# Performance work log

Measured on AMD Instinct MI355X. Metric: run time of the kernel, lower is better.

## Reference

```python
import jax, jax.numpy as jnp
import numpy as np

B, N, S, NS, V = 4, 4096, 1024, 32, 8
CIN, COUT = 64, 128
RADIUS = 0.2
C1 = CIN + 6  # cin + grouped_xyz(3) + local_xyz(3)
EPS = 1e-5


def _bn(x, g, b):
    # training-mode batchnorm over all axes except the trailing channel axis
    axes = tuple(range(x.ndim - 1))
    m = jnp.mean(x, axes, keepdims=True)
    v = jnp.var(x, axes, keepdims=True)
    return (x - m) * jax.lax.rsqrt(v + EPS) * g + b


def _fps(xyz, s):
    # farthest point sampling, deterministic start at index 0
    b, n, _ = xyz.shape
    bar = jnp.arange(b)
    def step(carry, _):
        mind, last = carry
        p = xyz[bar, last]  # [B,3]
        d = jnp.sum((xyz - p[:, None, :]) ** 2, -1)
        mind = jnp.minimum(mind, d)
        nxt = jnp.argmax(mind, -1).astype(jnp.int32)
        return (mind, nxt), nxt
    idx0 = jnp.zeros((b,), jnp.int32)
    _, rest = jax.lax.scan(step, (jnp.full((b, n), 1e10, xyz.dtype), idx0), None, length=s - 1)
    idx = jnp.concatenate([idx0[None], rest], 0).T  # [B,S]
    return jnp.take_along_axis(xyz, idx[..., None], axis=1), idx


def _ball_query(new_xyz, xyz, k, radius):
    # first-k-in-index-order points within radius; -1 padding like pytorch3d
    n = xyz.shape[1]
    d2 = jnp.sum((new_xyz[:, :, None, :] - xyz[:, None, :, :]) ** 2, -1)  # [B,S,N]
    key = jnp.where(d2 < radius * radius, jnp.arange(n, dtype=jnp.int32), n)
    negk, _ = jax.lax.top_k(-key, k)  # k smallest keys
    idx = -negk
    mask = idx >= n
    return jnp.where(mask, -1, idx), mask


def _masked_gather(x, idx):
    # gather rows of x [B,N,C] at idx [B,S,k]; zeros where idx == -1
    b, s, k = idx.shape
    safe = jnp.maximum(idx, 0).reshape(b, s * k)
    g = jnp.take_along_axis(x, safe[..., None], axis=1).reshape(b, s, k, x.shape[-1])
    return jnp.where((idx == -1)[..., None], 0.0, g)


def setup_inputs() -> dict:
    key = jax.random.key(0)
    ks = jax.random.split(key, 10)
    xyz = jax.random.uniform(ks[0], (B, N, 3), jnp.float32)
    f = jax.random.normal(ks[1], (B, N, CIN), jnp.float32)
    # cube-corner frame points, scaled by radius*0.8, rotated about Y (as in __init__)
    corners = jnp.array([[x, y, z] for x in (-1.0, 1.0) for y in (-1.0, 1.0) for z in (-1.0, 1.0)], jnp.float32)
    ang = jax.random.uniform(ks[2], ()) * 2.0 * jnp.pi
    c, sn = jnp.cos(ang), jnp.sin(ang)
    z, o = jnp.zeros(()), jnp.ones(())
    rot = jnp.stack([jnp.stack([c, z, sn]), jnp.stack([z, o, z]), jnp.stack([-sn, z, c])])
    framepoints = (corners * (RADIUS * 0.8)) @ rot.T
    w = lambda k_, sh: jax.random.normal(k_, sh, jnp.float32) * 0.05
    return {
        "xyz": xyz, "f": f, "framepoints": framepoints,
        "w1_0": w(ks[3], (13, 64)), "b1_0": jnp.zeros((64,), jnp.float32),
        "g1_0": jnp.ones((64,), jnp.float32), "bt1_0": jnp.zeros((64,), jnp.float32),
        "w1_1": w(ks[4], (64, C1)), "b1_1": jnp.zeros((C1,), jnp.float32),
        "w2_0": w(ks[5], (C1, 128)), "b2_0": jnp.zeros((128,), jnp.float32),
        "g2_0": jnp.ones((128,), jnp.float32), "bt2_0": jnp.zeros((128,), jnp.float32),
        "w2_1": w(ks[6], (128, COUT)), "b2_1": jnp.zeros((COUT,), jnp.float32),
        "res_w": w(ks[7], (CIN, COUT)), "res_b": jnp.zeros((COUT,), jnp.float32),
    }


def _forward(xyz, f, framepoints, w1_0, b1_0, g1_0, bt1_0, w1_1, b1_1,
             w2_0, b2_0, g2_0, bt2_0, w2_1, b2_1, res_w, res_b):
    new_xyz, _ = _fps(xyz, S)                           # [B,S,3]
    idx, mask = _ball_query(new_xyz, xyz, NS, RADIUS)   # [B,S,NS]
    grouped_xyz = _masked_gather(xyz, idx)              # [B,S,NS,3]
    grouped_feature = _masked_gather(f, idx)            # [B,S,NS,CIN]
    local = grouped_xyz - new_xyz[:, :, None, :]
    gf = jnp.concatenate([grouped_xyz, local, grouped_feature], -1)   # [B,S,NS,C1]
    arrow = grouped_xyz[:, :, :, None, :] - framepoints               # [B,S,NS,V,3]
    euc = jnp.sqrt(jnp.sum(arrow ** 2, -1, keepdims=True))
    gx = jnp.broadcast_to(grouped_xyz[:, :, :, None, :], arrow.shape)
    fp = jnp.broadcast_to(framepoints, arrow.shape)
    coc = jnp.concatenate([-arrow, arrow, euc, gx, fp], -1)           # [B,S,NS,V,13]
    # m1: per-point MLP (1x1x1 Conv3d) 13 -> 64 (bn+relu) -> C1
    a = jax.nn.relu(_bn(coc @ w1_0 + b1_0, g1_0, bt1_0))
    a = a @ w1_1 + b1_1                                               # [B,S,NS,V,C1]
    # frame-modulated features + softmax attention over the V frame axis
    p = gf[:, :, :, None, :] * a                                      # [B,S,NS,V,C1]
    agg = jnp.sum(jax.nn.softmax(p, axis=3) * p, axis=3)              # [B,S,NS,C1]
    agg = jnp.where(mask[..., None], 0.0, agg)
    # m2: per-point MLP (1x1 Conv2d) C1 -> 128 (bn+relu) -> COUT
    wmid = jax.nn.relu(_bn(agg @ w2_0 + b2_0, g2_0, bt2_0))
    wout = wmid @ w2_1 + b2_1                                         # [B,S,NS,COUT]
    new_f = jax.nn.gelu(wout + grouped_feature @ res_w + res_b, approximate=False)
    return jnp.max(new_f, axis=2), new_xyz


def reference(xyz, f, framepoints, w1_0, b1_0, g1_0, bt1_0, w1_1, b1_1,
              w2_0, b2_0, g2_0, bt2_0, w2_1, b2_1, res_w, res_b):
    return _forward(xyz, f, framepoints, w1_0, b1_0, g1_0, bt1_0, w1_1, b1_1,
                    w2_0, b2_0, g2_0, bt2_0, w2_1, b2_1, res_w, res_b)
```

## Files before the change

kernel.cpp:

```cpp
#include <hip/hip_runtime.h>
#include <hip/hip_bf16.h>
#include <math.h>

typedef __hip_bfloat16 bf16;
typedef __attribute__((ext_vector_type(8))) short short8;
typedef __attribute__((ext_vector_type(4))) float f32x4;

#define BB  4
#define NN  4096
#define SS  1024
#define KNS 32
#define C1  70

__device__ __forceinline__ float b2f(bf16 x){ return __bfloat162float(x); }

__device__ __forceinline__ float ld(const void* p, size_t i, bool F){
    return F ? ((const float*)p)[i] : __bfloat162float(((const bf16*)p)[i]);
}
__device__ __forceinline__ void st(void* p, size_t i, float v, bool F){
    if (F) ((float*)p)[i] = v; else ((bf16*)p)[i] = __float2bfloat16(v);
}
__device__ __forceinline__ unsigned short f2us(float x){
    __hip_bfloat16 h = __float2bfloat16(x);
    return *reinterpret_cast<unsigned short*>(&h);
}
__device__ __forceinline__ float us2f(unsigned short u){
    return __uint_as_float(((unsigned)u) << 16);
}

__global__ void init_kernel(const void* xyz, double* __restrict__ M,
                            double* __restrict__ sums, int* __restrict__ flag){
    __shared__ int cnt;
    const int t = threadIdx.x;
    if (t == 0) cnt = 0;
    if (t < 105) M[t] = 0.0;
    if (t < 256) sums[t] = 0.0;
    __syncthreads();
    int c = 0;
    for (int i = t; i < 2048; i += 256){
        float v = __bfloat162float(((const bf16*)xyz)[i]);
        if (!(fabsf(v) <= 1.5f)) c++;
    }
    atomicAdd(&cnt, c);
    __syncthreads();
    if (t == 0) *flag = (cnt > 10) ? 1 : 0;
}

__global__ __launch_bounds__(256) void fps_kernel(const void* __restrict__ xyz,
        float* __restrict__ nxf, void* __restrict__ out, const int* __restrict__ flag){
    __shared__ float4 pts[NN];
    __shared__ int sidx[SS];
    __shared__ unsigned long long skey[2][4];
    const bool F = (*flag != 0);
    const int b = blockIdx.x, t = threadIdx.x, lane = t & 63, w = t >> 6;
    float px[16], py[16], pz[16], mind[16];
#pragma unroll
    for (int j = 0; j < 16; j++){
        int i = j*256 + t;
        float X = ld(xyz, (size_t)(b*NN+i)*3+0, F);
        float Y = ld(xyz, (size_t)(b*NN+i)*3+1, F);
        float Z = ld(xyz, (size_t)(b*NN+i)*3+2, F);
        px[j] = X; py[j] = Y; pz[j] = Z; mind[j] = 1e10f;
        pts[i] = make_float4(X, Y, Z, 0.f);
    }
    if (t == 0) sidx[0] = 0;
    __syncthreads();
    float4 q = pts[0];
    for (int s = 1; s < SS; s++){
        float bd = -1.f; int bi = 0;
#pragma unroll
        for (int j = 0; j < 16; j++){
            float dx = __fsub_rn(px[j], q.x);
            float dy = __fsub_rn(py[j], q.y);
            float dz = __fsub_rn(pz[j], q.z);
            float d  = __fadd_rn(__fadd_rn(__fmul_rn(dx,dx), __fmul_rn(dy,dy)), __fmul_rn(dz,dz));
            float m = fminf(mind[j], d); mind[j] = m;
            if (m > bd){ bd = m; bi = j*256 + t; }
        }
        unsigned long long key = ((unsigned long long)__float_as_uint(bd) << 32)
                               | (unsigned)(~bi);
#pragma unroll
        for (int off = 1; off < 64; off <<= 1){
            unsigned long long o = __shfl_xor(key, off);
            if (o > key) key = o;
        }
        const int par = s & 1;
        if (lane == 0) skey[par][w] = key;
        __syncthreads();
        unsigned long long k0 = skey[par][0], k1 = skey[par][1];
        unsigned long long k2 = skey[par][2], k3 = skey[par][3];
        if (k1 > k0) k0 = k1;
        if (k3 > k2) k2 = k3;
        if (k2 > k0) k0 = k2;
        int ix = (int)(~(unsigned)(k0 & 0xffffffffull));
        if (t == 0) sidx[s] = ix;
        q = pts[ix];
    }
    __syncthreads();
    const size_t o1 = (size_t)BB*SS*128;
    for (int s2 = t; s2 < SS; s2 += 256){
        int i = sidx[s2];
        float4 p = pts[i];
        nxf[(b*SS+s2)*3+0] = p.x; nxf[(b*SS+s2)*3+1] = p.y; nxf[(b*SS+s2)*3+2] = p.z;
        st(out, o1 + (size_t)(b*SS+s2)*3+0, p.x, F);
        st(out, o1 + (size_t)(b*SS+s2)*3+1, p.y, F);
        st(out, o1 + (size_t)(b*SS+s2)*3+2, p.z, F);
    }
}

__global__ __launch_bounds__(512) void ball_kernel(const void* __restrict__ xyz,
        const float* __restrict__ nxf, int* __restrict__ idx, const int* __restrict__ flag){
    __shared__ float sx[NN], sy[NN], sz[NN];
    const bool F = (*flag != 0);
    const int b = blockIdx.x, t = threadIdx.x, lane = t & 63, w = t >> 6;
    for (int i = t; i < NN; i += 512){
        sx[i] = ld(xyz, (size_t)(b*NN+i)*3+0, F);
        sy[i] = ld(xyz, (size_t)(b*NN+i)*3+1, F);
        sz[i] = ld(xyz, (size_t)(b*NN+i)*3+2, F);
    }
    __syncthreads();
    const float R2 = 0.2f*0.2f;
    const unsigned long long below = (lane == 63) ? ~0ull >> 1
                                   : ((1ull << lane) - 1ull);
#pragma unroll
    for (int cc = 0; cc < 4; cc++){
        const int s = blockIdx.y*32 + w*4 + cc;
        const float px = nxf[(b*SS+s)*3+0];
        const float py = nxf[(b*SS+s)*3+1];
        const float pz = nxf[(b*SS+s)*3+2];
        int* op = idx + (size_t)(b*SS+s)*KNS;
        int cnt = 0;
        for (int c = 0; c < 64; c++){
            const int i = c*64 + lane;
            float dx = __fsub_rn(px, sx[i]);
            float dy = __fsub_rn(py, sy[i]);
            float dz = __fsub_rn(pz, sz[i]);
            float d2 = __fadd_rn(__fadd_rn(__fmul_rn(dx,dx), __fmul_rn(dy,dy)), __fmul_rn(dz,dz));
            const bool hit = (d2 < R2);
            unsigned long long m = __ballot(hit);
            if (hit){
                int pos = cnt + __popcll(m & below);
                if (pos < KNS) op[pos] = i;
            }
            cnt += __popcll(m);
            if (cnt >= KNS) break;
        }
        if (lane < KNS && lane >= cnt) op[lane] = -1;
    }
}

__global__ __launch_bounds__(256) void bn1_stats(const void* __restrict__ xyz,
        const int* __restrict__ idx, const void* __restrict__ fpt, double* __restrict__ M,
        const int* __restrict__ flag){
    __shared__ float sfp[24];
    const bool F = (*flag != 0);
    const int t = threadIdx.x, lane = t & 63;
    if (t < 24) sfp[t] = ld(fpt, t, F);
    __syncthreads();
    float acc[105];
#pragma unroll
    for (int q = 0; q < 105; q++) acc[q] = 0.f;
    for (int it = 0; it < 8; it++){
        const int row = blockIdx.x*2048 + it*256 + t;
        const int b = row >> 15;
        const int id = idx[row];
        float gx = 0.f, gy = 0.f, gz = 0.f;
        if (id >= 0){
            gx = ld(xyz, (size_t)(b*NN+id)*3+0, F);
            gy = ld(xyz, (size_t)(b*NN+id)*3+1, F);
            gz = ld(xyz, (size_t)(b*NN+id)*3+2, F);
        }
#pragma unroll
        for (int v = 0; v < 8; v++){
            float fxv = sfp[v*3+0], fyv = sfp[v*3+1], fzv = sfp[v*3+2];
            float ax = gx - fxv, ay = gy - fyv, az = gz - fzv;
            float eu = sqrtf(ax*ax + ay*ay + az*az);
            float fv[14];
            fv[0] = -ax; fv[1] = -ay; fv[2] = -az;
            fv[3] =  ax; fv[4] =  ay; fv[5] =  az;
            fv[6] = eu;  fv[7] = gx;  fv[8] = gy; fv[9] = gz;
            fv[10] = fxv; fv[11] = fyv; fv[12] = fzv; fv[13] = 1.0f;
            int q = 0;
#pragma unroll
            for (int i = 0; i < 14; i++)
#pragma unroll
                for (int j = i; j < 14; j++){
                    acc[q] = fmaf(fv[i], fv[j], acc[q]);
                    q++;
                }
        }
    }
#pragma unroll
    for (int q = 0; q < 105; q++){
        float s = acc[q];
#pragma unroll
        for (int off = 1; off < 64; off <<= 1) s += __shfl_xor(s, off);
        if (lane == 0) atomicAdd(&M[q], (double)s);
    }
}

__global__ __launch_bounds__(128) void bn1_final(const double* __restrict__ M,
        const void* __restrict__ w10, const void* __restrict__ b10,
        const void* __restrict__ g1, const void* __restrict__ bt1, float* __restrict__ bn1,
        const int* __restrict__ flag){
    __shared__ double Mm[14][14];
    __shared__ double mv[14];
    const bool F = (*flag != 0);
    const int t = threadIdx.x;
    if (t < 105){
        int e = t, i = 0, off = 0;
        while (e - off >= 14 - i){ off += 14 - i; i++; }
        int j = i + (e - off);
        double val = M[t];
        Mm[i][j] = val; Mm[j][i] = val;
    }
    __syncthreads();
    const double K = 1048576.0;
    if (t < 14) mv[t] = Mm[t][13] / K;
    __syncthreads();
    if (t < 64){
        double wc[13];
        for (int i = 0; i < 13; i++) wc[i] = (double)ld(w10, i*64+t, F);
        double mean = (double)ld(b10, t, F);
        for (int i = 0; i < 13; i++) mean += mv[i]*wc[i];
        double var = 0.0;
        for (int i = 0; i < 13; i++)
            for (int j = 0; j < 13; j++)
                var += wc[i]*wc[j]*(Mm[i][j]/K - mv[i]*mv[j]);
        float sc = ld(g1, t, F) / sqrtf((float)var + 1e-5f);
        bn1[t] = sc;
        bn1[64+t] = ld(bt1, t, F) - (float)mean * sc;
    }
}

__global__ __launch_bounds__(256) void m1_kernel(
        const void* __restrict__ xyz, const void* __restrict__ f, const void* __restrict__ fpt,
        const void* __restrict__ w10, const void* __restrict__ b10,
        const void* __restrict__ w11, const void* __restrict__ b11,
        const float* __restrict__ nxf, const int* __restrict__ idx,
        const float* __restrict__ bn1, float* __restrict__ agg, const int* __restrict__ flag){
    __shared__ short sthi[4*2*8*72];
    __shared__ short stlo[4*2*8*72];
    __shared__ float gfb[4*2*80];
    const bool F = (*flag != 0);
    const int t = threadIdx.x, lane = t & 63, w = t >> 6;
    const int kq = lane >> 4, cn = lane & 15;

    short8 Bh[2][5], Bl[2][5];
#pragma unroll
    for (int ks = 0; ks < 2; ks++)
#pragma unroll
    for (int nt = 0; nt < 5; nt++){
        short8 bh, bl;
#pragma unroll
        for (int j = 0; j < 8; j++){
            int k = ks*32 + kq*8 + j;
            int c = nt*16 + cn;
            float wv = (c < C1) ? ld(w11, (size_t)k*C1 + c, F) : 0.f;
            unsigned short h = f2us(wv);
            unsigned short l2 = f2us(wv - us2f(h));
            bh[j] = (short)h; bl[j] = (short)l2;
        }
        Bh[ks][nt] = bh; Bl[ks][nt] = bl;
    }
    float binit[5];
#pragma unroll
    for (int nt = 0; nt < 5; nt++){
        int c = nt*16 + cn;
        binit[nt] = (c < C1) ? ld(b11, c, F) : 0.f;
    }
    float W10c[13];
#pragma unroll
    for (int i = 0; i < 13; i++) W10c[i] = ld(w10, i*64+lane, F);
    const float b10v = ld(b10, lane, F);
    const float sc1 = bn1[lane], sh1 = bn1[64+lane];
    float fx[8], fy[8], fz[8];
#pragma unroll
    for (int v = 0; v < 8; v++){
        fx[v] = ld(fpt, v*3+0, F); fy[v] = ld(fpt, v*3+1, F); fz[v] = ld(fpt, v*3+2, F);
    }
    const int quad = lane >> 4;
    const int rr = quad >> 1;
    const int hh = quad & 1;
    const int mA = lane & 15;
    const int rA = mA >> 3, vA = mA & 7;

    const int wid = blockIdx.x*4 + w;
    for (int p = 0; p < 16; p++){
        const int rowbase = wid*32 + p*2;
        int ids[2];
#pragma unroll
        for (int r = 0; r < 2; r++){
            const int row = rowbase + r;
            const int b = row >> 15, s = (row >> 5) & 1023;
            const int id = idx[row];
            ids[r] = id;
            float gx = 0.f, gy = 0.f, gz = 0.f, fv0 = 0.f, fv1 = 0.f;
            if (id >= 0){
                gx = ld(xyz, (size_t)(b*NN+id)*3+0, F);
                gy = ld(xyz, (size_t)(b*NN+id)*3+1, F);
                gz = ld(xyz, (size_t)(b*NN+id)*3+2, F);
                if (lane >= 6) fv0 = ld(f, (size_t)(b*NN+id)*64 + (lane-6), F);
                if (lane < 6)  fv1 = ld(f, (size_t)(b*NN+id)*64 + (58+lane), F);
            }
            const float nxx = nxf[(b*SS+s)*3+0], nxy = nxf[(b*SS+s)*3+1], nxz = nxf[(b*SS+s)*3+2];
            float gf0;
            if (lane == 0) gf0 = gx; else if (lane == 1) gf0 = gy; else if (lane == 2) gf0 = gz;
            else if (lane == 3) gf0 = gx - nxx; else if (lane == 4) gf0 = gy - nxy;
            else if (lane == 5) gf0 = gz - nxz; else gf0 = fv0;
            gfb[w*160 + r*80 + lane] = gf0;
            if (lane < 6)       gfb[w*160 + r*80 + 64 + lane] = fv1;
            else if (lane < 16) gfb[w*160 + r*80 + 64 + lane] = 0.f;
            const int sb = ((w*2 + r)*8)*72 + lane;
#pragma unroll
            for (int v = 0; v < 8; v++){
                float ax = gx - fx[v], ay = gy - fy[v], az = gz - fz[v];
                float eu = sqrtf(ax*ax + ay*ay + az*az);
                float z = b10v;
                z = fmaf(-ax, W10c[0], z); z = fmaf(-ay, W10c[1], z); z = fmaf(-az, W10c[2], z);
                z = fmaf( ax, W10c[3], z); z = fmaf( ay, W10c[4], z); z = fmaf( az, W10c[5], z);
                z = fmaf( eu, W10c[6], z);
                z = fmaf( gx, W10c[7], z); z = fmaf( gy, W10c[8], z); z = fmaf( gz, W10c[9], z);
                z = fmaf(fx[v], W10c[10], z); z = fmaf(fy[v], W10c[11], z); z = fmaf(fz[v], W10c[12], z);
                float a1 = fmaxf(fmaf(z, sc1, sh1), 0.f);
                unsigned short h = f2us(a1);
                unsigned short l2 = f2us(a1 - us2f(h));
                sthi[sb + v*72] = (short)h;
                stlo[sb + v*72] = (short)l2;
            }
        }
        f32x4 acc[5];
#pragma unroll
        for (int nt = 0; nt < 5; nt++){
            f32x4 a; a[0] = binit[nt]; a[1] = binit[nt]; a[2] = binit[nt]; a[3] = binit[nt];
            acc[nt] = a;
        }
        const int aoff = ((w*2 + rA)*8 + vA)*72 + kq*8;
#pragma unroll
        for (int ks = 0; ks < 2; ks++){
            short8 ahi = *(const short8*)&sthi[aoff + ks*32];
            short8 alo = *(const short8*)&stlo[aoff + ks*32];
#pragma unroll
            for (int nt = 0; nt < 5; nt++){
                acc[nt] = __builtin_amdgcn_mfma_f32_16x16x32_bf16(ahi, Bh[ks][nt], acc[nt], 0, 0, 0);
                acc[nt] = __builtin_amdgcn_mfma_f32_16x16x32_bf16(alo, Bh[ks][nt], acc[nt], 0, 0, 0);
                acc[nt] = __builtin_amdgcn_mfma_f32_16x16x32_bf16(ahi, Bl[ks][nt], acc[nt], 0, 0, 0);
            }
        }
        const bool msk = ((rr == 0 ? ids[0] : ids[1]) < 0);
#pragma unroll
        for (int nt = 0; nt < 5; nt++){
            const int col = nt*16 + cn;
            float gfv = gfb[w*160 + rr*80 + col];
            f32x4 a = acc[nt];
            float p0 = a[0]*gfv, p1 = a[1]*gfv, p2 = a[2]*gfv, p3 = a[3]*gfv;
            float mx = fmaxf(fmaxf(p0, p1), fmaxf(p2, p3));
            mx = fmaxf(mx, __shfl_xor(mx, 16));
            float e0 = __expf(p0 - mx), e1 = __expf(p1 - mx);
            float e2 = __expf(p2 - mx), e3 = __expf(p3 - mx);
            float den4 = (e0 + e1) + (e2 + e3);
            float num4 = fmaf(e3, p3, fmaf(e2, p2, fmaf(e1, p1, e0*p0)));
            float den = den4 + __shfl_xor(den4, 16);
            float num = num4 + __shfl_xor(num4, 16);
            float outv = num / den;
            if (hh == 0 && col < C1){
                agg[(size_t)(rowbase + rr)*C1 + col] = msk ? 0.f : outv;
            }
        }
    }
}

__global__ __launch_bounds__(256) void prep1_kernel(
        const void* __restrict__ w20, const void* __restrict__ w21,
        const void* __restrict__ rw, const void* __restrict__ b20,
        const void* __restrict__ b21, const void* __restrict__ rb,
        float* __restrict__ w20r, float* __restrict__ w21f, float* __restrict__ rwf,
        float* __restrict__ b20r, float* __restrict__ bof, const int* __restrict__ flag){
    const bool F = (*flag != 0);
    int e = blockIdx.x*256 + threadIdx.x;
    if (e < 8960){ w20r[e] = ld(w20, e, F); return; }
    int e2 = e - 8960;
    if (e2 < 16384){ w21f[e2] = ld(w21, e2, F); return; }
    int e3 = e2 - 16384;
    if (e3 < 8192){ rwf[e3] = ld(rw, e3, F); return; }
    int e4 = e3 - 8192;
    if (e4 < 128){
        b20r[e4] = ld(b20, e4, F);
        bof[e4]  = ld(b21, e4, F) + ld(rb, e4, F);
    }
}

__global__ __launch_bounds__(256) void bn2_stats(const float* __restrict__ agg,
        const float* __restrict__ w20r, const float* __restrict__ b20r,
        double* __restrict__ sums){
    __shared__ float aggT[70*65];
    const int t = threadIdx.x, lane = t & 63;
    const int wbase = __builtin_amdgcn_readfirstlane((t >> 6) << 5);
    float binit[32];
#pragma unroll
    for (int j = 0; j < 32; j++) binit[j] = b20r[wbase + j];
    float accs[32], accq[32];
#pragma unroll
    for (int j = 0; j < 32; j++){ accs[j] = 0.f; accq[j] = 0.f; }
    for (int it = 0; it < 8; it++){
        const int rowbase = blockIdx.x*512 + it*64;
        __syncthreads();
        for (int e = t; e < 70*64; e += 256){
            int r = e / 70, k = e - r*70;
            aggT[k*65 + r] = agg[(size_t)rowbase*70 + e];
        }
        __syncthreads();
        float z[32];
#pragma unroll
        for (int j = 0; j < 32; j++) z[j] = binit[j];
#pragma unroll 2
        for (int k = 0; k < 70; k++){
            float av = aggT[k*65 + lane];
            const float* wr = w20r + k*128 + wbase;
#pragma unroll
            for (int j = 0; j < 32; j++) z[j] = fmaf(av, wr[j], z[j]);
        }
#pragma unroll
        for (int j = 0; j < 32; j++){
            accs[j] += z[j];
            accq[j] = fmaf(z[j], z[j], accq[j]);
        }
    }
#pragma unroll
    for (int j = 0; j < 32; j++){
        float s = accs[j], q = accq[j];
#pragma unroll
        for (int off = 1; off < 64; off <<= 1){
            s += __shfl_xor(s, off);
            q += __shfl_xor(q, off);
        }
        if (lane == 0){
            atomicAdd(&sums[wbase + j], (double)s);
            atomicAdd(&sums[128 + wbase + j], (double)q);
        }
    }
}

__global__ void bn2_final(const double* __restrict__ sums, const void* __restrict__ g2,
        const void* __restrict__ bt2, float* __restrict__ bn2, const int* __restrict__ flag){
    const bool F = (*flag != 0);
    int t = threadIdx.x;
    const double K = 131072.0;
    double mean = sums[t] / K;
    double var = sums[128+t] / K - mean*mean;
    float sc = ld(g2, t, F) / sqrtf((float)var + 1e-5f);
    bn2[t] = sc;
    bn2[128+t] = ld(bt2, t, F) - (float)mean * sc;
}

__global__ __launch_bounds__(256) void prep2_kernel(
        const float* __restrict__ w20r, const float* __restrict__ b20r,
        const float* __restrict__ bn2,
        float* __restrict__ w20f, float* __restrict__ b20f){
    int e = blockIdx.x*256 + threadIdx.x;
    if (e < 8960){ w20f[e] = w20r[e] * bn2[e & 127]; return; }
    int e2 = e - 8960;
    if (e2 < 128){ b20f[e2] = b20r[e2]*bn2[e2] + bn2[128+e2]; }
}

__global__ __launch_bounds__(256) void final_kernel(
        const float* __restrict__ agg, const void* __restrict__ f, const int* __restrict__ idx,
        const float* __restrict__ w20f, const float* __restrict__ b20f,
        const float* __restrict__ w21f, const float* __restrict__ rwf,
        const float* __restrict__ bof,
        void* __restrict__ out, const int* __restrict__ flag){
    __shared__ float aggT[70*65];
    __shared__ float gfs[64*65];
    __shared__ float wmids[128*64];
    __shared__ float obuf[256];
    const bool F = (*flag != 0);
    const int t = threadIdx.x, lane = t & 63;
    const int wbase = __builtin_amdgcn_readfirstlane((t >> 6) << 5);
    const int rowbase = blockIdx.x * 64;
    for (int e = t; e < 70*64; e += 256){
        int r = e / 70, k = e - r*70;
        aggT[k*65 + r] = agg[(size_t)rowbase*70 + e];
    }
    for (int e = t; e < 64*64; e += 256){
        int r = e >> 6, cin = e & 63;
        int id = idx[rowbase + r];
        int b = (rowbase + r) >> 15;
        gfs[cin*65 + r] = (id >= 0) ? ld(f, (size_t)(b*NN+id)*64 + cin, F) : 0.f;
    }
    __syncthreads();
    float acc[32];
#pragma unroll
    for (int j = 0; j < 32; j++) acc[j] = b20f[wbase + j];
#pragma unroll 2
    for (int k = 0; k < 70; k++){
        float av = aggT[k*65 + lane];
        const float* wr = w20f + k*128 + wbase;
#pragma unroll
        for (int j = 0; j < 32; j++) acc[j] = fmaf(av, wr[j], acc[j]);
    }
#pragma unroll
    for (int j = 0; j < 32; j++)
        wmids[(wbase + j)*64 + lane] = fmaxf(acc[j], 0.f);
    __syncthreads();
    float acc2[32];
#pragma unroll
    for (int j = 0; j < 32; j++) acc2[j] = bof[wbase + j];
#pragma unroll 2
    for (int k = 0; k < 128; k++){
        float wv = wmids[k*64 + lane];
        const float* wr = w21f + k*128 + wbase;
#pragma unroll
        for (int j = 0; j < 32; j++) acc2[j] = fmaf(wv, wr[j], acc2[j]);
    }
#pragma unroll 2
    for (int k = 0; k < 64; k++){
        float gv = gfs[k*65 + lane];
        const float* wr = rwf + k*128 + wbase;
#pragma unroll
        for (int j = 0; j < 32; j++) acc2[j] = fmaf(gv, wr[j], acc2[j]);
    }
#pragma unroll
    for (int j = 0; j < 32; j++){
        float x = acc2[j];
        float y = 0.5f * x * (1.f + erff(x * 0.70710678118654752f));
#pragma unroll
        for (int off = 1; off < 32; off <<= 1)
            y = fmaxf(y, __shfl_xor(y, off));
        if ((lane & 31) == 0) obuf[(lane >> 5)*128 + wbase + j] = y;
    }
    __syncthreads();
    st(out, (size_t)blockIdx.x*256 + t, obuf[t], F);
}

extern "C" void kernel_launch(void* const* d_in, const int* in_sizes, int n_in,
                              void* d_out, int out_size, void* d_ws, size_t ws_size,
                              hipStream_t stream){
    const void* xyz = d_in[0];
    const void* f   = d_in[1];
    const void* fpt = d_in[2];
    const void* w10 = d_in[3];
    const void* b10 = d_in[4];
    const void* g1  = d_in[5];
    const void* bt1 = d_in[6];
    const void* w11 = d_in[7];
    const void* b11 = d_in[8];
    const void* w20 = d_in[9];
    const void* b20 = d_in[10];
    const void* g2  = d_in[11];
    const void* bt2 = d_in[12];
    const void* w21 = d_in[13];
    const void* b21 = d_in[14];
    const void* rw  = d_in[15];
    const void* rb  = d_in[16];

    char* ws = (char*)d_ws;
    float*  nxf  = (float*) (ws + 0);
    int*    idx  = (int*)   (ws + 65536);
    double* M    = (double*)(ws + 655360);
    float*  bn1  = (float*) (ws + 786432);
    double* sums = (double*)(ws + 917504);
    float*  bn2  = (float*) (ws + 1048576);
    int*    flag = (int*)   (ws + 1050624);
    float*  w20f = (float*) (ws + 1114112);
    float*  w21f = (float*) (ws + 1179648);
    float*  rwf  = (float*) (ws + 1245184);
    float*  b20f = (float*) (ws + 1277952);
    float*  bof  = (float*) (ws + 1278464);
    float*  w20r = (float*) (ws + 1310720);
    float*  b20r = (float*) (ws + 1441792);
    float*  agg  = (float*) (ws + 2097152);

    init_kernel<<<1, 256, 0, stream>>>(xyz, M, sums, flag);
    fps_kernel<<<4, 256, 0, stream>>>(xyz, nxf, d_out, flag);
    ball_kernel<<<dim3(4, 32), 512, 0, stream>>>(xyz, nxf, idx, flag);
    prep1_kernel<<<132, 256, 0, stream>>>(w20, w21, rw, b20, b21, rb,
                                          w20r, w21f, rwf, b20r, bof, flag);
    bn1_stats<<<64, 256, 0, stream>>>(xyz, idx, fpt, M, flag);
    bn1_final<<<1, 128, 0, stream>>>(M, w10, b10, g1, bt1, bn1, flag);
    m1_kernel<<<1024, 256, 0, stream>>>(xyz, f, fpt, w10, b10, w11, b11, nxf, idx, bn1, agg, flag);
    bn2_stats<<<256, 256, 0, stream>>>(agg, w20r, b20r, sums);
    bn2_final<<<1, 128, 0, stream>>>(sums, g2, bt2, bn2, flag);
    prep2_kernel<<<36, 256, 0, stream>>>(w20r, b20r, bn2, w20f, b20f);
    final_kernel<<<2048, 256, 0, stream>>>(agg, f, idx, w20f, b20f, w21f, rwf, bof, d_out, flag);
}
```

Baseline: 1.467 ms.

## Move bn2_stats and final MLP GEMMs to split-bf16 MFMA, shrink bn1 moments

The fp32 scalar FMA GEMMs in bn2_stats and final_kernel become 16x16x32 bf16 MFMA ops. Each fp32 operand is split into hi and lo bf16 parts and three products are summed, keeping near-fp32 accuracy. Weights are pre-packed into MFMA fragment layout in prep1/prep2. bn1_stats now accumulates a deduplicated 11-feature second-moment matrix instead of 14, with signs remapped in bn1_final, and uses more blocks with fewer rows each. The cost is three MFMAs per tile and bf16-split rounding error.

```diff
diff --git a/kernel.cpp b/kernel.cpp
--- a/kernel.cpp
+++ b/kernel.cpp
@@ -157,11 +157,11 @@
     const int t = threadIdx.x, lane = t & 63;
     if (t < 24) sfp[t] = ld(fpt, t, F);
     __syncthreads();
-    float acc[105];
-#pragma unroll
-    for (int q = 0; q < 105; q++) acc[q] = 0.f;
-    for (int it = 0; it < 8; it++){
-        const int row = blockIdx.x*2048 + it*256 + t;
+    float acc[66];
+#pragma unroll
+    for (int q = 0; q < 66; q++) acc[q] = 0.f;
+    for (int it = 0; it < 4; it++){
+        const int row = blockIdx.x*1024 + it*256 + t;
         const int b = row >> 15;
         const int id = idx[row];
         float gx = 0.f, gy = 0.f, gz = 0.f;
@@ -175,23 +175,22 @@
             float fxv = sfp[v*3+0], fyv = sfp[v*3+1], fzv = sfp[v*3+2];
             float ax = gx - fxv, ay = gy - fyv, az = gz - fzv;
             float eu = sqrtf(ax*ax + ay*ay + az*az);
-            float fv[14];
-            fv[0] = -ax; fv[1] = -ay; fv[2] = -az;
-            fv[3] =  ax; fv[4] =  ay; fv[5] =  az;
-            fv[6] = eu;  fv[7] = gx;  fv[8] = gy; fv[9] = gz;
-            fv[10] = fxv; fv[11] = fyv; fv[12] = fzv; fv[13] = 1.0f;
+            float f11[11];
+            f11[0] = ax; f11[1] = ay; f11[2] = az; f11[3] = eu;
+            f11[4] = gx; f11[5] = gy; f11[6] = gz;
+            f11[7] = fxv; f11[8] = fyv; f11[9] = fzv; f11[10] = 1.0f;
             int q = 0;
 #pragma unroll
-            for (int i = 0; i < 14; i++)
-#pragma unroll
-                for (int j = i; j < 14; j++){
-                    acc[q] = fmaf(fv[i], fv[j], acc[q]);
+            for (int i = 0; i < 11; i++)
+#pragma unroll
+                for (int j = i; j < 11; j++){
+                    acc[q] = fmaf(f11[i], f11[j], acc[q]);
                     q++;
                 }
         }
     }
 #pragma unroll
-    for (int q = 0; q < 105; q++){
+    for (int q = 0; q < 66; q++){
         float s = acc[q];
 #pragma unroll
         for (int off = 1; off < 64; off <<= 1) s += __shfl_xor(s, off);
@@ -203,30 +202,34 @@
         const void* __restrict__ w10, const void* __restrict__ b10,
         const void* __restrict__ g1, const void* __restrict__ bt1, float* __restrict__ bn1,
         const int* __restrict__ flag){
-    __shared__ double Mm[14][14];
-    __shared__ double mv[14];
+    __shared__ double Ms[11][11];
+    __shared__ double mv14[14];
     const bool F = (*flag != 0);
     const int t = threadIdx.x;
-    if (t < 105){
+    if (t < 66){
         int e = t, i = 0, off = 0;
-        while (e - off >= 14 - i){ off += 14 - i; i++; }
+        while (e - off >= 11 - i){ off += 11 - i; i++; }
         int j = i + (e - off);
         double val = M[t];
-        Mm[i][j] = val; Mm[j][i] = val;
+        Ms[i][j] = val; Ms[j][i] = val;
     }
     __syncthreads();
     const double K = 1048576.0;
-    if (t < 14) mv[t] = Mm[t][13] / K;
+    const int    bi14[14] = {0,1,2, 0,1,2, 3, 4,5,6, 7,8,9, 10};
+    const double sg14[14] = {-1,-1,-1, 1,1,1, 1, 1,1,1, 1,1,1, 1};
+    if (t < 14) mv14[t] = sg14[t] * Ms[bi14[t]][10] / K;
     __syncthreads();
     if (t < 64){
         double wc[13];
         for (int i = 0; i < 13; i++) wc[i] = (double)ld(w10, i*64+t, F);
         double mean = (double)ld(b10, t, F);
-        for (int i = 0; i < 13; i++) mean += mv[i]*wc[i];
+        for (int i = 0; i < 13; i++) mean += mv14[i]*wc[i];
         double var = 0.0;
         for (int i = 0; i < 13; i++)
-            for (int j = 0; j < 13; j++)
-                var += wc[i]*wc[j]*(Mm[i][j]/K - mv[i]*mv[j]);
+            for (int j = 0; j < 13; j++){
+                double mij = sg14[i]*sg14[j]*Ms[bi14[i]][bi14[j]]/K;
+                var += wc[i]*wc[j]*(mij - mv14[i]*mv14[j]);
+            }
         float sc = ld(g1, t, F) / sqrtf((float)var + 1e-5f);
         bn1[t] = sc;
         bn1[64+t] = ld(bt1, t, F) - (float)mean * sc;
@@ -370,73 +373,107 @@
     }
 }
 
+__device__ __forceinline__ void pack_frag(int e, int K, const void* W, bool F, float scale,
+                                          short* H, short* L){
+    int j = e & 7, lane = (e >> 3) & 63, nt = (e >> 9) & 7, kt = e >> 12;
+    int k = kt*32 + ((lane >> 4) & 3)*8 + j;
+    int n = nt*16 + (lane & 15);
+    float v = (k < K) ? ld(W, (size_t)k*128 + n, F) * scale : 0.f;
+    unsigned short h = f2us(v);
+    unsigned short l2 = f2us(v - us2f(h));
+    H[e] = (short)h; L[e] = (short)l2;
+}
+
 __global__ __launch_bounds__(256) void prep1_kernel(
         const void* __restrict__ w20, const void* __restrict__ w21,
         const void* __restrict__ rw, const void* __restrict__ b20,
         const void* __restrict__ b21, const void* __restrict__ rb,
-        float* __restrict__ w20r, float* __restrict__ w21f, float* __restrict__ rwf,
+        short* __restrict__ w20rp_h, short* __restrict__ w20rp_l,
+        short* __restrict__ w21p_h, short* __restrict__ w21p_l,
+        short* __restrict__ rwp_h, short* __restrict__ rwp_l,
         float* __restrict__ b20r, float* __restrict__ bof, const int* __restrict__ flag){
     const bool F = (*flag != 0);
     int e = blockIdx.x*256 + threadIdx.x;
-    if (e < 8960){ w20r[e] = ld(w20, e, F); return; }
-    int e2 = e - 8960;
-    if (e2 < 16384){ w21f[e2] = ld(w21, e2, F); return; }
-    int e3 = e2 - 16384;
-    if (e3 < 8192){ rwf[e3] = ld(rw, e3, F); return; }
-    int e4 = e3 - 8192;
-    if (e4 < 128){
-        b20r[e4] = ld(b20, e4, F);
-        bof[e4]  = ld(b21, e4, F) + ld(rb, e4, F);
+    if (e < 12288){ pack_frag(e, 70, w20, F, 1.f, w20rp_h, w20rp_l); return; }
+    e -= 12288;
+    if (e < 16384){ pack_frag(e, 128, w21, F, 1.f, w21p_h, w21p_l); return; }
+    e -= 16384;
+    if (e < 8192){ pack_frag(e, 64, rw, F, 1.f, rwp_h, rwp_l); return; }
+    e -= 8192;
+    if (e < 128){
+        b20r[e] = ld(b20, e, F);
+        bof[e]  = ld(b21, e, F) + ld(rb, e, F);
     }
 }
 
 __global__ __launch_bounds__(256) void bn2_stats(const float* __restrict__ agg,
-        const float* __restrict__ w20r, const float* __restrict__ b20r,
-        double* __restrict__ sums){
-    __shared__ float aggT[70*65];
-    const int t = threadIdx.x, lane = t & 63;
-    const int wbase = __builtin_amdgcn_readfirstlane((t >> 6) << 5);
-    float binit[32];
-#pragma unroll
-    for (int j = 0; j < 32; j++) binit[j] = b20r[wbase + j];
-    float accs[32], accq[32];
-#pragma unroll
-    for (int j = 0; j < 32; j++){ accs[j] = 0.f; accq[j] = 0.f; }
+        const short* __restrict__ w20rp_h, const short* __restrict__ w20rp_l,
+        const float* __restrict__ b20r, double* __restrict__ sums){
+    __shared__ short Xh[64*104];
+    __shared__ short Xl[64*104];
+    const int t = threadIdx.x, lane = t & 63, w = t >> 6;
+    const int cn = lane & 15, kq = lane >> 4;
+    for (int e = t; e < 64*34; e += 256){
+        int r = e/34, k = 70 + (e - r*34);
+        Xh[r*104+k] = 0; Xl[r*104+k] = 0;
+    }
+    float bias[8];
+#pragma unroll
+    for (int nt = 0; nt < 8; nt++) bias[nt] = b20r[nt*16 + cn];
+    f32x4 accS[8], accQ[8];
+#pragma unroll
+    for (int nt = 0; nt < 8; nt++){
+        f32x4 zz; zz[0]=0.f; zz[1]=0.f; zz[2]=0.f; zz[3]=0.f;
+        accS[nt] = zz; accQ[nt] = zz;
+    }
     for (int it = 0; it < 8; it++){
         const int rowbase = blockIdx.x*512 + it*64;
         __syncthreads();
-        for (int e = t; e < 70*64; e += 256){
-            int r = e / 70, k = e - r*70;
-            aggT[k*65 + r] = agg[(size_t)rowbase*70 + e];
+        for (int e = t; e < 64*70; e += 256){
+            int r = e/70, k = e - r*70;
+            float v = agg[(size_t)rowbase*70 + e];
+            unsigned short h = f2us(v);
+            unsigned short l2 = f2us(v - us2f(h));
+            Xh[r*104+k] = (short)h; Xl[r*104+k] = (short)l2;
         }
         __syncthreads();
-        float z[32];
-#pragma unroll
-        for (int j = 0; j < 32; j++) z[j] = binit[j];
-#pragma unroll 2
-        for (int k = 0; k < 70; k++){
-            float av = aggT[k*65 + lane];
-            const float* wr = w20r + k*128 + wbase;
-#pragma unroll
-            for (int j = 0; j < 32; j++) z[j] = fmaf(av, wr[j], z[j]);
-        }
-#pragma unroll
-        for (int j = 0; j < 32; j++){
-            accs[j] += z[j];
-            accq[j] = fmaf(z[j], z[j], accq[j]);
-        }
-    }
-#pragma unroll
-    for (int j = 0; j < 32; j++){
-        float s = accs[j], q = accq[j];
-#pragma unroll
-        for (int off = 1; off < 64; off <<= 1){
-            s += __shfl_xor(s, off);
-            q += __shfl_xor(q, off);
-        }
-        if (lane == 0){
-            atomicAdd(&sums[wbase + j], (double)s);
-            atomicAdd(&sums[128 + wbase + j], (double)q);
+        f32x4 z[8];
+#pragma unroll
+        for (int nt = 0; nt < 8; nt++){
+            f32x4 a; a[0]=bias[nt]; a[1]=bias[nt]; a[2]=bias[nt]; a[3]=bias[nt];
+            z[nt] = a;
+        }
+#pragma unroll
+        for (int kt = 0; kt < 3; kt++){
+            short8 Ah = *(const short8*)&Xh[(w*16 + cn)*104 + kt*32 + kq*8];
+            short8 Al = *(const short8*)&Xl[(w*16 + cn)*104 + kt*32 + kq*8];
+#pragma unroll
+            for (int nt = 0; nt < 8; nt++){
+                short8 Wh = ((const short8*)w20rp_h)[(kt*8+nt)*64 + lane];
+                short8 Wl = ((const short8*)w20rp_l)[(kt*8+nt)*64 + lane];
+                z[nt] = __builtin_amdgcn_mfma_f32_16x16x32_bf16(Ah, Wh, z[nt], 0, 0, 0);
+                z[nt] = __builtin_amdgcn_mfma_f32_16x16x32_bf16(Al, Wh, z[nt], 0, 0, 0);
+                z[nt] = __builtin_amdgcn_mfma_f32_16x16x32_bf16(Ah, Wl, z[nt], 0, 0, 0);
+            }
+        }
+#pragma unroll
+        for (int nt = 0; nt < 8; nt++){
+#pragma unroll
+            for (int rg = 0; rg < 4; rg++){
+                accS[nt][rg] += z[nt][rg];
+                accQ[nt][rg] = fmaf(z[nt][rg], z[nt][rg], accQ[nt][rg]);
+            }
+        }
+    }
+#pragma unroll
+    for (int nt = 0; nt < 8; nt++){
+        float s = (accS[nt][0] + accS[nt][1]) + (accS[nt][2] + accS[nt][3]);
+        float q = (accQ[nt][0] + accQ[nt][1]) + (accQ[nt][2] + accQ[nt][3]);
+        s += __shfl_xor(s, 16); s += __shfl_xor(s, 32);
+        q += __shfl_xor(q, 16); q += __shfl_xor(q, 32);
+        if (lane < 16){
+            atomicAdd(&sums[nt*16 + cn], (double)s);
+            atomicAdd(&sums[128 + nt*16 + cn], (double)q);
         }
     }
 }
@@ -454,82 +491,149 @@
 }
 
 __global__ __launch_bounds__(256) void prep2_kernel(
-        const float* __restrict__ w20r, const float* __restrict__ b20r,
+        const void* __restrict__ w20, const float* __restrict__ b20r,
         const float* __restrict__ bn2,
-        float* __restrict__ w20f, float* __restrict__ b20f){
+        short* __restrict__ w20p_h, short* __restrict__ w20p_l,
+        float* __restrict__ b20f, const int* __restrict__ flag){
+    const bool F = (*flag != 0);
     int e = blockIdx.x*256 + threadIdx.x;
-    if (e < 8960){ w20f[e] = w20r[e] * bn2[e & 127]; return; }
-    int e2 = e - 8960;
-    if (e2 < 128){ b20f[e2] = b20r[e2]*bn2[e2] + bn2[128+e2]; }
+    if (e < 12288){
+        int j = e & 7, lane = (e >> 3) & 63, nt = (e >> 9) & 7, kt = e >> 12;
+        int k = kt*32 + ((lane >> 4) & 3)*8 + j;
+        int n = nt*16 + (lane & 15);
+        float v = (k < 70) ? ld(w20, (size_t)k*128 + n, F) * bn2[n] : 0.f;
+        unsigned short h = f2us(v);
+        unsigned short l2 = f2us(v - us2f(h));
+        w20p_h[e] = (short)h; w20p_l[e] = (short)l2;
+        return;
+    }
+    e -= 12288;
+    if (e < 128) b20f[e] = b20r[e]*bn2[e] + bn2[128+e];
 }
 
 __global__ __launch_bounds__(256) void final_kernel(
         const float* __restrict__ agg, const void* __restrict__ f, const int* __restrict__ idx,
-        const float* __restrict__ w20f, const float* __restrict__ b20f,
-        const float* __restrict__ w21f, const float* __restrict__ rwf,
+        const short* __restrict__ w20p_h, const short* __restrict__ w20p_l,
+        const float* __restrict__ b20f,
+        const short* __restrict__ w21p_h, const short* __restrict__ w21p_l,
+        const short* __restrict__ rwp_h, const short* __restrict__ rwp_l,
         const float* __restrict__ bof,
         void* __restrict__ out, const int* __restrict__ flag){
-    __shared__ float aggT[70*65];
-    __shared__ float gfs[64*65];
-    __shared__ float wmids[128*64];
-    __shared__ float obuf[256];
-    const bool F = (*flag != 0);
-    const int t = threadIdx.x, lane = t & 63;
-    const int wbase = __builtin_amdgcn_readfirstlane((t >> 6) << 5);
+    __shared__ short Xh[64*104];
+    __shared__ short Xl[64*104];
+    __shared__ short Yh[64*152];
+    __shared__ short Yl[64*152];
+    __shared__ float obuf[4][128];
+    const bool F = (*flag != 0);
+    const int t = threadIdx.x, lane = t & 63, w = t >> 6;
+    const int cn = lane & 15, kq = lane >> 4;
     const int rowbase = blockIdx.x * 64;
-    for (int e = t; e < 70*64; e += 256){
-        int r = e / 70, k = e - r*70;
-        aggT[k*65 + r] = agg[(size_t)rowbase*70 + e];
+    for (int e = t; e < 64*34; e += 256){
+        int r = e/34, k = 70 + (e - r*34);
+        Xh[r*104+k] = 0; Xl[r*104+k] = 0;
+    }
+    for (int e = t; e < 64*70; e += 256){
+        int r = e/70, k = e - r*70;
+        float v = agg[(size_t)rowbase*70 + e];
+        unsigned short h = f2us(v);
+        unsigned short l2 = f2us(v - us2f(h));
+        Xh[r*104+k] = (short)h; Xl[r*104+k] = (short)l2;
+    }
+    __syncthreads();
+    f32x4 z[8];
+#pragma unroll
+    for (int nt = 0; nt < 8; nt++){
+        float b = b20f[nt*16 + cn];
+        f32x4 a; a[0]=b; a[1]=b; a[2]=b; a[3]=b;
+        z[nt] = a;
+    }
+#pragma unroll
+    for (int kt = 0; kt < 3; kt++){
+        short8 Ah = *(const short8*)&Xh[(w*16 + cn)*104 + kt*32 + kq*8];
+        short8 Al = *(const short8*)&Xl[(w*16 + cn)*104 + kt*32 + kq*8];
+#pragma unroll
+        for (int nt = 0; nt < 8; nt++){
+            short8 Wh = ((const short8*)w20p_h)[(kt*8+nt)*64 + lane];
+            short8 Wl = ((const short8*)w20p_l)[(kt*8+nt)*64 + lane];
+            z[nt] = __builtin_amdgcn_mfma_f32_16x16x32_bf16(Ah, Wh, z[nt], 0, 0, 0);
+            z[nt] = __builtin_amdgcn_mfma_f32_16x16x32_bf16(Al, Wh, z[nt], 0, 0, 0);
+            z[nt] = __builtin_amdgcn_mfma_f32_16x16x32_bf16(Ah, Wl, z[nt], 0, 0, 0);
+        }
+    }
+    __syncthreads();
+#pragma unroll
+    for (int nt = 0; nt < 8; nt++){
+#pragma unroll
+        for (int rg = 0; rg < 4; rg++){
+            float y = fmaxf(z[nt][rg], 0.f);
+            unsigned short h = f2us(y);
+            unsigned short l2 = f2us(y - us2f(h));
+            int row = w*16 + kq*4 + rg, col = nt*16 + cn;
+            Yh[row*152+col] = (short)h; Yl[row*152+col] = (short)l2;
+        }
     }
     for (int e = t; e < 64*64; e += 256){
-        int r = e >> 6, cin = e & 63;
+        int r = e >> 6, k = e & 63;
         int id = idx[rowbase + r];
         int b = (rowbase + r) >> 15;
-        gfs[cin*65 + r] = (id >= 0) ? ld(f, (size_t)(b*NN+id)*64 + cin, F) : 0.f;
-    }
-    __syncthreads();
-    float acc[32];
-#pragma unroll
-    for (int j = 0; j < 32; j++) acc[j] = b20f[wbase + j];
-#pragma unroll 2
-    for (int k = 0; k < 70; k++){
-        float av = aggT[k*65 + lane];
-        const float* wr = w20f + k*128 + wbase;
-#pragma unroll
-        for (int j = 0; j < 32; j++) acc[j] = fmaf(av, wr[j], acc[j]);
-    }
-#pragma unroll
-    for (int j = 0; j < 32; j++)
-        wmids[(wbase + j)*64 + lane] = fmaxf(acc[j], 0.f);
-    __syncthreads();
-    float acc2[32];
-#pragma unroll
-    for (int j = 0; j < 32; j++) acc2[j] = bof[wbase + j];
-#pragma unroll 2
-    for (int k = 0; k < 128; k++){
-        float wv = wmids[k*64 + lane];
-        const float* wr = w21f + k*128 + wbase;
-#pragma unroll
-        for (int j = 0; j < 32; j++) acc2[j] = fmaf(wv, wr[j], acc2[j]);
-    }
-#pragma unroll 2
-    for (int k = 0; k < 64; k++){
-        float gv = gfs[k*65 + lane];
-        const float* wr = rwf + k*128 + wbase;
-#pragma unroll
-        for (int j = 0; j < 32; j++) acc2[j] = fmaf(gv, wr[j], acc2[j]);
-    }
-#pragma unroll
-    for (int j = 0; j < 32; j++){
-        float x = acc2[j];
-        float y = 0.5f * x * (1.f + erff(x * 0.70710678118654752f));
-#pragma unroll
-        for (int off = 1; off < 32; off <<= 1)
-            y = fmaxf(y, __shfl_xor(y, off));
-        if ((lane & 31) == 0) obuf[(lane >> 5)*128 + wbase + j] = y;
-    }
-    __syncthreads();
-    st(out, (size_t)blockIdx.x*256 + t, obuf[t], F);
+        float v = (id >= 0) ? ld(f, (size_t)(b*NN+id)*64 + k, F) : 0.f;
+        unsigned short h = f2us(v);
+        unsigned short l2 = f2us(v - us2f(h));
+        Xh[r*88+k] = (short)h; Xl[r*88+k] = (short)l2;
+    }
+    __syncthreads();
+    f32x4 acc2[8];
+#pragma unroll
+    for (int nt = 0; nt < 8; nt++){
+        float b = bof[nt*16 + cn];
+        f32x4 a; a[0]=b; a[1]=b; a[2]=b; a[3]=b;
+        acc2[nt] = a;
+    }
+#pragma unroll
+    for (int kt = 0; kt < 4; kt++){
+        short8 Ah = *(const short8*)&Yh[(w*16 + cn)*152 + kt*32 + kq*8];
+        short8 Al = *(const short8*)&Yl[(w*16 + cn)*152 + kt*32 + kq*8];
+#pragma unroll
+        for (int nt = 0; nt < 8; nt++){
+            short8 Wh = ((const short8*)w21p_h)[(kt*8+nt)*64 + lane];
+            short8 Wl = ((const short8*)w21p_l)[(kt*8+nt)*64 + lane];
+            acc2[nt] = __builtin_amdgcn_mfma_f32_16x16x32_bf16(Ah, Wh, acc2[nt], 0, 0, 0);
+            acc2[nt] = __builtin_amdgcn_mfma_f32_16x16x32_bf16(Al, Wh, acc2[nt], 0, 0, 0);
+            acc2[nt] = __builtin_amdgcn_mfma_f32_16x16x32_bf16(Ah, Wl, acc2[nt], 0, 0, 0);
+        }
+    }
+#pragma unroll
+    for (int kt = 0; kt < 2; kt++){
+        short8 Ah = *(const short8*)&Xh[(w*16 + cn)*88 + kt*32 + kq*8];
+        short8 Al = *(const short8*)&Xl[(w*16 + cn)*88 + kt*32 + kq*8];
+#pragma unroll
+        for (int nt = 0; nt < 8; nt++){
+            short8 Wh = ((const short8*)rwp_h)[(kt*8+nt)*64 + lane];
+            short8 Wl = ((const short8*)rwp_l)[(kt*8+nt)*64 + lane];
+            acc2[nt] = __builtin_amdgcn_mfma_f32_16x16x32_bf16(Ah, Wh, acc2[nt], 0, 0, 0);
+            acc2[nt] = __builtin_amdgcn_mfma_f32_16x16x32_bf16(Al, Wh, acc2[nt], 0, 0, 0);
+            acc2[nt] = __builtin_amdgcn_mfma_f32_16x16x32_bf16(Ah, Wl, acc2[nt], 0, 0, 0);
+        }
+    }
+#pragma unroll
+    for (int nt = 0; nt < 8; nt++){
+        float m = -3.4e38f;
+#pragma unroll
+        for (int rg = 0; rg < 4; rg++){
+            float x = acc2[nt][rg];
+            float y = 0.5f * x * (1.f + erff(x * 0.70710678118654752f));
+            m = fmaxf(m, y);
+        }
+        m = fmaxf(m, __shfl_xor(m, 16));
+        m = fmaxf(m, __shfl_xor(m, 32));
+        if (lane < 16) obuf[w][nt*16 + cn] = m;
+    }
+    __syncthreads();
+    {
+        int g = t >> 7, c = t & 127;
+        float y = fmaxf(obuf[2*g][c], obuf[2*g+1][c]);
+        st(out, (size_t)blockIdx.x*256 + t, y, F);
+    }
 }
 
 extern "C" void kernel_launch(void* const* d_in, const int* in_sizes, int n_in,
@@ -554,32 +658,38 @@
     const void* rb  = d_in[16];
 
     char* ws = (char*)d_ws;
-    float*  nxf  = (float*) (ws + 0);
-    int*    idx  = (int*)   (ws + 65536);
-    double* M    = (double*)(ws + 655360);
-    float*  bn1  = (float*) (ws + 786432);
-    double* sums = (double*)(ws + 917504);
-    float*  bn2  = (float*) (ws + 1048576);
-    int*    flag = (int*)   (ws + 1050624);
-    float*  w20f = (float*) (ws + 1114112);
-    float*  w21f = (float*) (ws + 1179648);
-    float*  rwf  = (float*) (ws + 1245184);
-    float*  b20f = (float*) (ws + 1277952);
-    float*  bof  = (float*) (ws + 1278464);
-    float*  w20r = (float*) (ws + 1310720);
-    float*  b20r = (float*) (ws + 1441792);
-    float*  agg  = (float*) (ws + 2097152);
+    float*  nxf     = (float*) (ws + 0);
+    int*    idx     = (int*)   (ws + 65536);
+    double* M       = (double*)(ws + 655360);
+    float*  bn1     = (float*) (ws + 786432);
+    double* sums    = (double*)(ws + 917504);
+    float*  bn2     = (float*) (ws + 1048576);
+    int*    flag    = (int*)   (ws + 1050624);
+    float*  b20r    = (float*) (ws + 1060864);
+    float*  bof     = (float*) (ws + 1061376);
+    float*  b20f    = (float*) (ws + 1061888);
+    short*  w20rp_h = (short*) (ws + 1064960);
+    short*  w20rp_l = (short*) (ws + 1089536);
+    short*  w20p_h  = (short*) (ws + 1114112);
+    short*  w20p_l  = (short*) (ws + 1138688);
+    short*  w21p_h  = (short*) (ws + 1163264);
+    short*  w21p_l  = (short*) (ws + 1196032);
+    short*  rwp_h   = (short*) (ws + 1228800);
+    short*  rwp_l   = (short*) (ws + 1245184);
+    float*  agg     = (float*) (ws + 2097152);
 
     init_kernel<<<1, 256, 0, stream>>>(xyz, M, sums, flag);
     fps_kernel<<<4, 256, 0, stream>>>(xyz, nxf, d_out, flag);
     ball_kernel<<<dim3(4, 32), 512, 0, stream>>>(xyz, nxf, idx, flag);
-    prep1_kernel<<<132, 256, 0, stream>>>(w20, w21, rw, b20, b21, rb,
-                                          w20r, w21f, rwf, b20r, bof, flag);
-    bn1_stats<<<64, 256, 0, stream>>>(xyz, idx, fpt, M, flag);
+    prep1_kernel<<<145, 256, 0, stream>>>(w20, w21, rw, b20, b21, rb,
+                                          w20rp_h, w20rp_l, w21p_h, w21p_l,
+                                          rwp_h, rwp_l, b20r, bof, flag);
+    bn1_stats<<<128, 256, 0, stream>>>(xyz, idx, fpt, M, flag);
     bn1_final<<<1, 128, 0, stream>>>(M, w10, b10, g1, bt1, bn1, flag);
     m1_kernel<<<1024, 256, 0, stream>>>(xyz, f, fpt, w10, b10, w11, b11, nxf, idx, bn1, agg, flag);
-    bn2_stats<<<256, 256, 0, stream>>>(agg, w20r, b20r, sums);
+    bn2_stats<<<256, 256, 0, stream>>>(agg, w20rp_h, w20rp_l, b20r, sums);
     bn2_final<<<1, 128, 0, stream>>>(sums, g2, bt2, bn2, flag);
-    prep2_kernel<<<36, 256, 0, stream>>>(w20r, b20r, bn2, w20f, b20f);
-    final_kernel<<<2048, 256, 0, stream>>>(agg, f, idx, w20f, b20f, w21f, rwf, bof, d_out, flag);
-}
+    prep2_kernel<<<49, 256, 0, stream>>>(w20, b20r, bn2, w20p_h, w20p_l, b20f, flag);
+    final_kernel<<<2048, 256, 0, stream>>>(agg, f, idx, w20p_h, w20p_l, b20f,
+                                           w21p_h, w21p_l, rwp_h, rwp_l, bof, d_out, flag);
+}
```

Measured after the change: 1.357 ms. -7.5%, faster.
